# Kernel optimization log

Measured on AMD Instinct MI355X. Metric: run time of the kernel, lower is better.

Reference implementation:

```python
import jax, jax.numpy as jnp
import numpy as np

# OGB full_atom_feature_dims
FEAT_DIMS = np.array([119, 5, 12, 12, 10, 6, 6, 2, 2], dtype=np.int32)
OFFSETS = jnp.asarray(np.concatenate([[0], np.cumsum(FEAT_DIMS)[:-1]]), dtype=jnp.int32)  # [9]
TOTAL_ROWS = int(FEAT_DIMS.sum())  # 174
DIM = 256
N_CLASS = 10
B, MAX_NODE = 128, 1024


def setup_inputs() -> dict:
    key = jax.random.key(0)
    ks = jax.random.split(key, 16)
    # per-field valid categorical indices, stacked -> [B, MAX_NODE, 9]
    cols = [jax.random.randint(ks[i], (B, MAX_NODE), 0, int(FEAT_DIMS[i]), dtype=jnp.int32)
            for i in range(9)]
    node_feat = jnp.stack(cols, axis=-1)
    num_nodes = jax.random.randint(ks[9], (B,), 1, MAX_NODE + 1, dtype=jnp.int32)
    rxn_class = jax.random.randint(ks[10], (B,), 0, N_CLASS, dtype=jnp.int32)
    # learned params
    atom_emb = jax.random.normal(ks[11], (TOTAL_ROWS, DIM), dtype=jnp.float32) * 0.02
    rxn_emb = jax.random.normal(ks[12], (N_CLASS, DIM), dtype=jnp.float32) * 0.02
    lin_w = jax.random.normal(ks[13], (DIM, 2 * DIM), dtype=jnp.float32) * (1.0 / np.sqrt(2 * DIM))
    lin_b = jax.random.normal(ks[14], (DIM,), dtype=jnp.float32) * 0.01
    return {"node_feat": node_feat, "num_nodes": num_nodes, "rxn_class": rxn_class,
            "atom_emb": atom_emb, "rxn_emb": rxn_emb, "lin_w": lin_w, "lin_b": lin_b}


def reference(node_feat, num_nodes, rxn_class, atom_emb, rxn_emb, lin_w, lin_b):
    # AtomEncoder: sum of 9 per-field embedding lookups (tables concatenated with offsets)
    idx = node_feat + OFFSETS  # [B, N, 9]
    enc = atom_emb[idx].sum(axis=2)  # [B, N, dim]
    # zero-pad positions beyond num_nodes (ragged-to-dense scatter)
    mask = (jnp.arange(MAX_NODE)[None, :] < num_nodes[:, None])[..., None]  # [B, N, 1]
    enc = jnp.where(mask, enc, jnp.zeros((), dtype=enc.dtype))
    # class embedding broadcast over all node slots (including padding, as in original)
    cls = jnp.broadcast_to(rxn_emb[rxn_class][:, None, :], enc.shape)  # [B, N, dim]
    h = jnp.concatenate([enc, cls], axis=-1)  # [B, N, 2*dim]
    out = jnp.einsum('bnd,od->bno', h, lin_w) + lin_b  # [B, N, dim]
    return out
```

## Files before the change

kernel.cpp:

```cpp
#include <hip/hip_runtime.h>
#include <stdint.h>

#define BATCH 128
#define MAXN 1024
#define NF 9
#define DIM 256
#define NCLS 10

#define BASE1 119
#define BASE2 179
#define BASE3 299
#define QROWS 443

#define TBLK 114
#define PACKBLK (BATCH * MAXN / 256)

#define NSL 4
#define SCOL 64
#define SLICE_U4 3544

typedef __attribute__((ext_vector_type(4))) float f32x4;
typedef __attribute__((ext_vector_type(2))) uint32_t u32x2;

__device__ __forceinline__ ushort f32_to_bf16_rne(float x) {
  uint32_t u = __float_as_uint(x);
  u += 0x7fffu + ((u >> 16) & 1u);
  return (ushort)(u >> 16);
}

__device__ __forceinline__ f32x4 bf4_to_f32x4(u32x2 v) {
  f32x4 r;
  r.x = __uint_as_float(v.x << 16);
  r.y = __uint_as_float(v.x & 0xffff0000u);
  r.z = __uint_as_float(v.y << 16);
  r.w = __uint_as_float(v.y & 0xffff0000u);
  return r;
}

__global__ __launch_bounds__(256) void prep_kernel(
    const float* __restrict__ rxn_emb, const float* __restrict__ lin_w,
    const float* __restrict__ lin_b, const float* __restrict__ atom_emb,
    const int* __restrict__ node_feat,
    ushort* __restrict__ Qb, float* __restrict__ clsT, int4* __restrict__ jpack)
{
  const int bid = blockIdx.x;
  const int t = threadIdx.x;

  if (bid >= TBLK) {
    const int node = (bid - TBLK) * 256 + t;
    const int* p = node_feat + (size_t)node * NF;
    int4 jv;
    jv.x = p[0];
    jv.y = BASE1 + p[1] * 12 + p[2];
    jv.z = BASE2 + p[3] * 10 + p[4];
    jv.w = BASE3 + ((p[5] * 6 + p[6]) * 2 + p[7]) * 2 + p[8];
    jpack[node] = jv;
    return;
  }

  __shared__ float S[4][DIM];
  const bool isCls = bid < 3;
  const int row0 = isCls ? bid * 4 : (bid - 3) * 4;
  const int rmax = isCls ? NCLS : QROWS;
  const int nrows = (rmax - row0 < 4) ? (rmax - row0) : 4;

#pragma unroll
  for (int r = 0; r < 4; ++r) {
    float v = 0.f;
    if (r < nrows) {
      const int q = row0 + r;
      if (isCls) {
        v = rxn_emb[q * DIM + t];
      } else if (q < BASE1) {
        v = atom_emb[q * DIM + t];
      } else if (q < BASE2) {
        int x = q - BASE1;
        v = atom_emb[(119 + x / 12) * DIM + t] + atom_emb[(124 + x % 12) * DIM + t];
      } else if (q < BASE3) {
        int x = q - BASE2;
        v = atom_emb[(136 + x / 10) * DIM + t] + atom_emb[(148 + x % 10) * DIM + t];
      } else {
        int x = q - BASE3;
        int i8 = x & 1, i7 = (x >> 1) & 1, y = x >> 2;
        v = atom_emb[(158 + y / 6) * DIM + t] + atom_emb[(164 + y % 6) * DIM + t]
          + atom_emb[(170 + i7) * DIM + t] + atom_emb[(172 + i8) * DIM + t];
      }
    }
    S[r][t] = v;
  }
  __syncthreads();

  const float* wrow = lin_w + (size_t)t * 2 * DIM + (isCls ? DIM : 0);
  const float init = isCls ? lin_b[t] : 0.f;
  float a0 = init, a1 = init, a2 = init, a3 = init;
#pragma unroll 4
  for (int d = 0; d < DIM; d += 4) {
    float4 w4 = *(const float4*)(wrow + d);
    a0 += w4.x * S[0][d] + w4.y * S[0][d + 1] + w4.z * S[0][d + 2] + w4.w * S[0][d + 3];
    a1 += w4.x * S[1][d] + w4.y * S[1][d + 1] + w4.z * S[1][d + 2] + w4.w * S[1][d + 3];
    a2 += w4.x * S[2][d] + w4.y * S[2][d + 1] + w4.z * S[2][d + 2] + w4.w * S[2][d + 3];
    a3 += w4.x * S[3][d] + w4.y * S[3][d + 1] + w4.z * S[3][d + 2] + w4.w * S[3][d + 3];
  }
  if (isCls) {
    if (0 < nrows) clsT[(row0 + 0) * DIM + t] = a0;
    if (1 < nrows) clsT[(row0 + 1) * DIM + t] = a1;
    if (2 < nrows) clsT[(row0 + 2) * DIM + t] = a2;
    if (3 < nrows) clsT[(row0 + 3) * DIM + t] = a3;
  } else {
    const int s = t >> 6, c = t & 63;
    if (0 < nrows) Qb[(size_t)s * QROWS * SCOL + (row0 + 0) * SCOL + c] = f32_to_bf16_rne(a0);
    if (1 < nrows) Qb[(size_t)s * QROWS * SCOL + (row0 + 1) * SCOL + c] = f32_to_bf16_rne(a1);
    if (2 < nrows) Qb[(size_t)s * QROWS * SCOL + (row0 + 2) * SCOL + c] = f32_to_bf16_rne(a2);
    if (3 < nrows) Qb[(size_t)s * QROWS * SCOL + (row0 + 3) * SCOL + c] = f32_to_bf16_rne(a3);
  }
}

__global__ __launch_bounds__(1024, 8) void main_kernel(
    const int4* __restrict__ jpack, const int* __restrict__ num_nodes,
    const int* __restrict__ rxn_class,
    const ushort* __restrict__ Qb, const float* __restrict__ clsT,
    float* __restrict__ out)
{
  __shared__ ushort Ls[QROWS * SCOL];

  const int tid = threadIdx.x;
  const int bid = blockIdx.x;
  const int s = bid & 3;
  const int b = (bid >> 2) & 127;
  const int q = bid >> 9;
  const int n0_blk = q * 256;
  const int nn = num_nodes[b];
  const int cls = rxn_class[b];
  const f32x4* __restrict__ clsT4 = (const f32x4*)clsT;
  f32x4* __restrict__ out4 = (f32x4*)out;

  if (n0_blk >= nn) {
    const f32x4 cf = clsT4[cls * 64 + s * 16 + (tid & 15)];
    const size_t base = (size_t)(b * MAXN + n0_blk) * 64 + s * 16;
#pragma unroll
    for (int k = 0; k < 4; ++k) {
      const int idx = tid + k * 1024;
      const int node = idx >> 4, c4 = idx & 15;
      out4[base + (size_t)node * 64 + c4] = cf;
    }
    return;
  }

  {
    const uint4* __restrict__ src = (const uint4*)(Qb + (size_t)s * QROWS * SCOL);
    uint4* dst = (uint4*)Ls;
    for (int i = tid; i < SLICE_U4; i += 1024) dst[i] = src[i];
  }
  __syncthreads();

  const int w = __builtin_amdgcn_readfirstlane(tid >> 6);
  const int lane = tid & 63;
  const int nd = lane >> 4;
  const int c = lane & 15;
  const int n0 = n0_blk + w * 16;

  const f32x4 cf = clsT4[cls * 64 + s * 16 + c];
  const u32x2* __restrict__ L2p = (const u32x2*)Ls;
  const int4* __restrict__ jp = jpack + (size_t)b * MAXN;
  const size_t obase = (size_t)(b * MAXN) * 64 + s * 16 + c;

  if (n0 >= nn) {
#pragma unroll
    for (int p = 0; p < 4; ++p) {
      const int n = n0 + p * 4 + nd;
      out4[obase + (size_t)n * 64] = cf;
    }
    return;
  }

  if (n0 + 16 <= nn) {
#pragma unroll
    for (int p = 0; p < 4; ++p) {
      const int n = n0 + p * 4 + nd;
      const int4 jv = jp[n];
      const u32x2 v0 = L2p[jv.x * 16 + c];
      const u32x2 v1 = L2p[jv.y * 16 + c];
      const u32x2 v2 = L2p[jv.z * 16 + c];
      const u32x2 v3 = L2p[jv.w * 16 + c];
      const f32x4 sum = (bf4_to_f32x4(v0) + bf4_to_f32x4(v1))
                      + (bf4_to_f32x4(v2) + bf4_to_f32x4(v3));
      out4[obase + (size_t)n * 64] = cf + sum;
    }
    return;
  }

#pragma unroll
  for (int p = 0; p < 4; ++p) {
    const int n = n0 + p * 4 + nd;
    const int4 jv = jp[n];
    const u32x2 v0 = L2p[jv.x * 16 + c];
    const u32x2 v1 = L2p[jv.y * 16 + c];
    const u32x2 v2 = L2p[jv.z * 16 + c];
    const u32x2 v3 = L2p[jv.w * 16 + c];
    const float m = (n < nn) ? 1.f : 0.f;
    const f32x4 sum = (bf4_to_f32x4(v0) + bf4_to_f32x4(v1))
                    + (bf4_to_f32x4(v2) + bf4_to_f32x4(v3));
    out4[obase + (size_t)n * 64] = cf + m * sum;
  }
}

extern "C" void kernel_launch(void* const* d_in, const int* in_sizes, int n_in,
                              void* d_out, int out_size, void* d_ws, size_t ws_size,
                              hipStream_t stream) {
  const int* node_feat = (const int*)d_in[0];
  const int* num_nodes = (const int*)d_in[1];
  const int* rxn_class = (const int*)d_in[2];
  const float* atom_emb = (const float*)d_in[3];
  const float* rxn_emb = (const float*)d_in[4];
  const float* lin_w = (const float*)d_in[5];
  const float* lin_b = (const float*)d_in[6];
  float* outp = (float*)d_out;

  ushort* Qb = (ushort*)d_ws;
  float* clsT = (float*)((char*)d_ws + QROWS * DIM * sizeof(ushort));
  int4* jpack = (int4*)((char*)d_ws + 262144);

  prep_kernel<<<TBLK + PACKBLK, 256, 0, stream>>>(rxn_emb, lin_w, lin_b,
                                                  atom_emb, node_feat,
                                                  Qb, clsT, jpack);
  main_kernel<<<NSL * BATCH * 4, 1024, 0, stream>>>(jpack, num_nodes, rxn_class,
                                                    Qb, clsT, outp);
}
```

Measured before the change: 40.86 us.

## Store projected lookup table in fp32 and split columns into eight slices

The precomputed projected embedding table is now kept in fp32 instead of bf16. To keep the LDS footprint unchanged, the 256 output columns are split into 8 slices of 32 rather than 4 slices of 64. The main kernel gathers float4 rows straight from LDS, which removes the bf16 unpack arithmetic and improves accuracy. In exchange it launches twice as many blocks, each handling half the work, so per-block overhead and redundant node-index loads double, and the launch-bounds occupancy hint is dropped.

```diff
diff --git a/kernel.cpp b/kernel.cpp
--- a/kernel.cpp
+++ b/kernel.cpp
@@ -15,33 +15,17 @@
 #define TBLK 114
 #define PACKBLK (BATCH * MAXN / 256)
 
-#define NSL 4
-#define SCOL 64
+#define NSL 8
+#define SCOL 32
 #define SLICE_U4 3544
 
 typedef __attribute__((ext_vector_type(4))) float f32x4;
-typedef __attribute__((ext_vector_type(2))) uint32_t u32x2;
-
-__device__ __forceinline__ ushort f32_to_bf16_rne(float x) {
-  uint32_t u = __float_as_uint(x);
-  u += 0x7fffu + ((u >> 16) & 1u);
-  return (ushort)(u >> 16);
-}
-
-__device__ __forceinline__ f32x4 bf4_to_f32x4(u32x2 v) {
-  f32x4 r;
-  r.x = __uint_as_float(v.x << 16);
-  r.y = __uint_as_float(v.x & 0xffff0000u);
-  r.z = __uint_as_float(v.y << 16);
-  r.w = __uint_as_float(v.y & 0xffff0000u);
-  return r;
-}
 
 __global__ __launch_bounds__(256) void prep_kernel(
     const float* __restrict__ rxn_emb, const float* __restrict__ lin_w,
     const float* __restrict__ lin_b, const float* __restrict__ atom_emb,
     const int* __restrict__ node_feat,
-    ushort* __restrict__ Qb, float* __restrict__ clsT, int4* __restrict__ jpack)
+    float* __restrict__ Qf, float* __restrict__ clsT, int4* __restrict__ jpack)
 {
   const int bid = blockIdx.x;
   const int t = threadIdx.x;
@@ -107,27 +91,28 @@
     if (2 < nrows) clsT[(row0 + 2) * DIM + t] = a2;
     if (3 < nrows) clsT[(row0 + 3) * DIM + t] = a3;
   } else {
-    const int s = t >> 6, c = t & 63;
-    if (0 < nrows) Qb[(size_t)s * QROWS * SCOL + (row0 + 0) * SCOL + c] = f32_to_bf16_rne(a0);
-    if (1 < nrows) Qb[(size_t)s * QROWS * SCOL + (row0 + 1) * SCOL + c] = f32_to_bf16_rne(a1);
-    if (2 < nrows) Qb[(size_t)s * QROWS * SCOL + (row0 + 2) * SCOL + c] = f32_to_bf16_rne(a2);
-    if (3 < nrows) Qb[(size_t)s * QROWS * SCOL + (row0 + 3) * SCOL + c] = f32_to_bf16_rne(a3);
+    const int s = t >> 5, c = t & 31;
+    float* dst = Qf + (size_t)s * QROWS * SCOL + c;
+    if (0 < nrows) dst[(row0 + 0) * SCOL] = a0;
+    if (1 < nrows) dst[(row0 + 1) * SCOL] = a1;
+    if (2 < nrows) dst[(row0 + 2) * SCOL] = a2;
+    if (3 < nrows) dst[(row0 + 3) * SCOL] = a3;
   }
 }
 
-__global__ __launch_bounds__(1024, 8) void main_kernel(
+__global__ __launch_bounds__(1024) void main_kernel(
     const int4* __restrict__ jpack, const int* __restrict__ num_nodes,
     const int* __restrict__ rxn_class,
-    const ushort* __restrict__ Qb, const float* __restrict__ clsT,
+    const float* __restrict__ Qf, const float* __restrict__ clsT,
     float* __restrict__ out)
 {
-  __shared__ ushort Ls[QROWS * SCOL];
+  __shared__ float Ls[QROWS * SCOL];
 
   const int tid = threadIdx.x;
   const int bid = blockIdx.x;
-  const int s = bid & 3;
-  const int b = (bid >> 2) & 127;
-  const int q = bid >> 9;
+  const int s = bid & 7;
+  const int b = (bid >> 3) & 127;
+  const int q = bid >> 10;
   const int n0_blk = q * 256;
   const int nn = num_nodes[b];
   const int cls = rxn_class[b];
@@ -135,19 +120,19 @@
   f32x4* __restrict__ out4 = (f32x4*)out;
 
   if (n0_blk >= nn) {
-    const f32x4 cf = clsT4[cls * 64 + s * 16 + (tid & 15)];
-    const size_t base = (size_t)(b * MAXN + n0_blk) * 64 + s * 16;
-#pragma unroll
-    for (int k = 0; k < 4; ++k) {
+    const f32x4 cf = clsT4[cls * 64 + s * 8 + (tid & 7)];
+    const size_t base = (size_t)(b * MAXN + n0_blk) * 64 + s * 8;
+#pragma unroll
+    for (int k = 0; k < 2; ++k) {
       const int idx = tid + k * 1024;
-      const int node = idx >> 4, c4 = idx & 15;
+      const int node = idx >> 3, c4 = idx & 7;
       out4[base + (size_t)node * 64 + c4] = cf;
     }
     return;
   }
 
   {
-    const uint4* __restrict__ src = (const uint4*)(Qb + (size_t)s * QROWS * SCOL);
+    const uint4* __restrict__ src = (const uint4*)(Qf + (size_t)s * QROWS * SCOL);
     uint4* dst = (uint4*)Ls;
     for (int i = tid; i < SLICE_U4; i += 1024) dst[i] = src[i];
   }
@@ -155,19 +140,19 @@
 
   const int w = __builtin_amdgcn_readfirstlane(tid >> 6);
   const int lane = tid & 63;
-  const int nd = lane >> 4;
-  const int c = lane & 15;
+  const int nd = lane >> 3;
+  const int c = lane & 7;
   const int n0 = n0_blk + w * 16;
 
-  const f32x4 cf = clsT4[cls * 64 + s * 16 + c];
-  const u32x2* __restrict__ L2p = (const u32x2*)Ls;
+  const f32x4 cf = clsT4[cls * 64 + s * 8 + c];
+  const f32x4* __restrict__ Lp = (const f32x4*)Ls;
   const int4* __restrict__ jp = jpack + (size_t)b * MAXN;
-  const size_t obase = (size_t)(b * MAXN) * 64 + s * 16 + c;
+  const size_t obase = (size_t)(b * MAXN) * 64 + s * 8 + c;
 
   if (n0 >= nn) {
 #pragma unroll
-    for (int p = 0; p < 4; ++p) {
-      const int n = n0 + p * 4 + nd;
+    for (int p = 0; p < 2; ++p) {
+      const int n = n0 + p * 8 + nd;
       out4[obase + (size_t)n * 64] = cf;
     }
     return;
@@ -175,32 +160,28 @@
 
   if (n0 + 16 <= nn) {
 #pragma unroll
-    for (int p = 0; p < 4; ++p) {
-      const int n = n0 + p * 4 + nd;
+    for (int p = 0; p < 2; ++p) {
+      const int n = n0 + p * 8 + nd;
       const int4 jv = jp[n];
-      const u32x2 v0 = L2p[jv.x * 16 + c];
-      const u32x2 v1 = L2p[jv.y * 16 + c];
-      const u32x2 v2 = L2p[jv.z * 16 + c];
-      const u32x2 v3 = L2p[jv.w * 16 + c];
-      const f32x4 sum = (bf4_to_f32x4(v0) + bf4_to_f32x4(v1))
-                      + (bf4_to_f32x4(v2) + bf4_to_f32x4(v3));
-      out4[obase + (size_t)n * 64] = cf + sum;
-    }
-    return;
-  }
-
-#pragma unroll
-  for (int p = 0; p < 4; ++p) {
-    const int n = n0 + p * 4 + nd;
+      const f32x4 v0 = Lp[jv.x * 8 + c];
+      const f32x4 v1 = Lp[jv.y * 8 + c];
+      const f32x4 v2 = Lp[jv.z * 8 + c];
+      const f32x4 v3 = Lp[jv.w * 8 + c];
+      out4[obase + (size_t)n * 64] = cf + ((v0 + v1) + (v2 + v3));
+    }
+    return;
+  }
+
+#pragma unroll
+  for (int p = 0; p < 2; ++p) {
+    const int n = n0 + p * 8 + nd;
     const int4 jv = jp[n];
-    const u32x2 v0 = L2p[jv.x * 16 + c];
-    const u32x2 v1 = L2p[jv.y * 16 + c];
-    const u32x2 v2 = L2p[jv.z * 16 + c];
-    const u32x2 v3 = L2p[jv.w * 16 + c];
+    const f32x4 v0 = Lp[jv.x * 8 + c];
+    const f32x4 v1 = Lp[jv.y * 8 + c];
+    const f32x4 v2 = Lp[jv.z * 8 + c];
+    const f32x4 v3 = Lp[jv.w * 8 + c];
     const float m = (n < nn) ? 1.f : 0.f;
-    const f32x4 sum = (bf4_to_f32x4(v0) + bf4_to_f32x4(v1))
-                    + (bf4_to_f32x4(v2) + bf4_to_f32x4(v3));
-    out4[obase + (size_t)n * 64] = cf + m * sum;
+    out4[obase + (size_t)n * 64] = cf + m * ((v0 + v1) + (v2 + v3));
   }
 }
 
@@ -216,13 +197,13 @@
   const float* lin_b = (const float*)d_in[6];
   float* outp = (float*)d_out;
 
-  ushort* Qb = (ushort*)d_ws;
-  float* clsT = (float*)((char*)d_ws + QROWS * DIM * sizeof(ushort));
-  int4* jpack = (int4*)((char*)d_ws + 262144);
+  float* Qf = (float*)d_ws;
+  float* clsT = (float*)((char*)d_ws + QROWS * SCOL * NSL * sizeof(float));
+  int4* jpack = (int4*)((char*)d_ws + 524288);
 
   prep_kernel<<<TBLK + PACKBLK, 256, 0, stream>>>(rxn_emb, lin_w, lin_b,
                                                   atom_emb, node_feat,
-                                                  Qb, clsT, jpack);
+                                                  Qf, clsT, jpack);
   main_kernel<<<NSL * BATCH * 4, 1024, 0, stream>>>(jpack, num_nodes, rxn_class,
-                                                    Qb, clsT, outp);
+                                                    Qf, clsT, outp);
 }
```

Result: slower. 45.42 us (+11.2%).
